# Kernel tuning notes

Hardware: AMD Instinct MI355X
Metric: run time of the kernel (lower is better)

Reference implementation:

```python
import jax, jax.numpy as jnp
import numpy as np

N = 131072
MANO_CHILD = (2, 3, 17, 5, 6, 18, 8, 9, 20, 11, 12, 19, 14, 15, 16)
MANO_PARENT = (1, 2, 3, 4, 5, 6, 7, 8, 9, 10, 11, 12, 13, 14, 15)
FINGERS = ((0, 1, 2, 3, 17), (0, 4, 5, 6, 18), (0, 7, 8, 9, 20), (0, 10, 11, 12, 19), (0, 13, 14, 15, 16))
PALM = np.array([0, 1, 4, 7, 10, 13])
MAX_FLEX = float(np.pi / 2)  # flexion clamp range [0, pi/2]
EPS = 1e-8


def _wrist_rot(src, dst):
    """Kabsch rotation R (N,3,3) such that R @ src_k ~= dst_k (palm alignment)."""
    H = jnp.einsum('nki,nkj->nij', src, dst)          # sum_k src dst^T
    U, S, Vt = jnp.linalg.svd(H, full_matrices=False)
    VUt = jnp.einsum('nji,nkj->nik', Vt, U)           # V @ U^T
    d = jnp.linalg.det(VUt)
    D = jnp.stack([jnp.ones_like(d), jnp.ones_like(d), d], axis=-1)
    return jnp.einsum('nji,nj,nkj->nik', Vt, D, U)    # V diag(1,1,d) U^T


def _rodrigues(v, axis, theta):
    """Rotate vectors v (N,3) about unit axis (N,3) by angle theta (N,)."""
    c = jnp.cos(theta)[:, None]
    s = jnp.sin(theta)[:, None]
    return v * c + jnp.cross(axis, v) * s + axis * jnp.sum(axis * v, -1, keepdims=True) * (1.0 - c)


def _forward(joints, tempJ):
    wrist = joints[:, :1]
    J = joints - wrist                       # wrist-centered observed joints
    T = tempJ - tempJ[:, :1]                 # wrist-centered template
    bone_ref = T                             # bonelenTempJ: reference bone lengths
    # rigid palm alignment of template onto observed joints
    R = _wrist_rot(T[:, PALM], J[:, PALM])
    T = jnp.einsum('nij,nkj->nki', R, T)     # rotate every template joint
    # palm joints of observation are replaced by aligned template palm
    J = J.at[:, PALM].set(T[:, PALM])
    # (hand-pose-legitimize layer approximated as identity; source unavailable)
    for idx in range(len(MANO_CHILD)):
        ch, pa = MANO_CHILD[idx], MANO_PARENT[idx]
        v1 = J[:, ch] - T[:, pa]
        dis = jnp.linalg.norm(v1, axis=1)
        univ1 = v1 / (dis[:, None] + EPS)
        blen = jnp.linalg.norm(bone_ref[:, ch] - bone_ref[:, pa], axis=1)
        lo, hi = blen, blen                  # non-RHD template: lower == upper
        valid = (lo <= dis) & (dis <= hi)
        clamped = jnp.clip(dis, lo, hi)
        new = jnp.where(valid[:, None], J[:, ch], T[:, pa] + univ1 * clamped[:, None])
        T = T.at[:, ch].set(new)
        # flexion legitimization: clamp bend angle of this bone vs its parent bone
        f = FINGERS[idx // 3]
        k = idx % 3
        gp, pp, cc = f[k], f[k + 1], f[k + 2]  # grandparent, parent(=pa), child(=ch)
        v0 = T[:, pp] - T[:, gp]
        vb = T[:, cc] - T[:, pp]
        cr = jnp.cross(v0, vb)
        s = jnp.linalg.norm(cr, axis=1)
        c = jnp.sum(v0 * vb, axis=1)
        ang = jnp.arctan2(s, c)
        delta = jnp.clip(ang, 0.0, MAX_FLEX) - ang
        axis = cr / (s[:, None] + EPS)
        T = T.at[:, cc].set(_rodrigues(vb, axis, delta) + T[:, pp])
    return wrist + T


def setup_inputs() -> dict:
    key = jax.random.key(0)
    k1, k2 = jax.random.split(key)
    joints = jax.random.normal(k1, (N, 21, 3), dtype=jnp.float32)
    tempJ = jax.random.normal(k2, (N, 21, 3), dtype=jnp.float32)
    return {"joints": joints, "tempJ": tempJ}


def reference(joints, tempJ):
    return _forward(joints, tempJ)
```

## Files before the change

### kernel.cpp

```cpp
#include <hip/hip_runtime.h>
#include <math.h>

#define KEPS 1e-8f

__global__ __launch_bounds__(256)
void kin_fwd(const float* __restrict__ joints,
             const float* __restrict__ tempJ,
             float* __restrict__ out,
             int n_total)
{
    constexpr int CHILD[15]  = {2,3,17, 5,6,18, 8,9,20, 11,12,19, 14,15,16};
    constexpr int PARENT[15] = {1,2,3, 4,5,6, 7,8,9, 10,11,12, 13,14,15};
    constexpr int GPID[15]   = {0,1,2, 0,4,5, 0,7,8, 0,10,11, 0,13,14};
    constexpr int PALM[6]    = {0,1,4,7,10,13};

    const int n = blockIdx.x * blockDim.x + threadIdx.x;
    if (n >= n_total) return;

    const float* jp = joints + (long long)n * 63;
    const float* tp = tempJ  + (long long)n * 63;

    float Jl[21][3], T[21][3];
#pragma unroll
    for (int k = 0; k < 21; ++k) {
        Jl[k][0] = jp[3*k+0];
        Jl[k][1] = jp[3*k+1];
        Jl[k][2] = jp[3*k+2];
    }
    const float wx = Jl[0][0], wy = Jl[0][1], wz = Jl[0][2];
#pragma unroll
    for (int k = 0; k < 21; ++k) { Jl[k][0] -= wx; Jl[k][1] -= wy; Jl[k][2] -= wz; }

#pragma unroll
    for (int k = 0; k < 21; ++k) {
        T[k][0] = tp[3*k+0];
        T[k][1] = tp[3*k+1];
        T[k][2] = tp[3*k+2];
    }
    const float ox = T[0][0], oy = T[0][1], oz = T[0][2];
#pragma unroll
    for (int k = 0; k < 21; ++k) { T[k][0] -= ox; T[k][1] -= oy; T[k][2] -= oz; }

    float blen[15];
#pragma unroll
    for (int i = 0; i < 15; ++i) {
        const float dx = T[CHILD[i]][0] - T[PARENT[i]][0];
        const float dy = T[CHILD[i]][1] - T[PARENT[i]][1];
        const float dz = T[CHILD[i]][2] - T[PARENT[i]][2];
        blen[i] = sqrtf(dx*dx + dy*dy + dz*dz);
    }

    float H[3][3] = {{0.f,0.f,0.f},{0.f,0.f,0.f},{0.f,0.f,0.f}};
#pragma unroll
    for (int p = 0; p < 6; ++p) {
        const int k = PALM[p];
#pragma unroll
        for (int i = 0; i < 3; ++i)
#pragma unroll
            for (int j = 0; j < 3; ++j)
                H[i][j] += T[k][i] * Jl[k][j];
    }

    float A[3][3];
#pragma unroll
    for (int i = 0; i < 3; ++i)
#pragma unroll
        for (int j = 0; j < 3; ++j)
            A[i][j] = H[0][i]*H[0][j] + H[1][i]*H[1][j] + H[2][i]*H[2][j];

    float V[3][3] = {{1.f,0.f,0.f},{0.f,1.f,0.f},{0.f,0.f,1.f}};
#pragma unroll
    for (int sw = 0; sw < 6; ++sw) {
#pragma unroll
        for (int r = 0; r < 3; ++r) {
            const int p = (r == 2) ? 1 : 0;
            const int q = (r == 0) ? 1 : 2;
            const float b   = A[p][q];
            const float dif = A[q][q] - A[p][p];
            const float rho = sqrtf(dif*dif + 4.f*b*b);
            const float c2  = (rho > 0.f) ? (dif / rho) : 1.f;
            const float c   = sqrtf(fmaxf(0.5f*(1.f + c2), 0.f));
            const float s   = copysignf(sqrtf(fmaxf(0.5f*(1.f - c2), 0.f)), b);
#pragma unroll
            for (int i = 0; i < 3; ++i) {
                const float aip = A[i][p], aiq = A[i][q];
                A[i][p] = c*aip - s*aiq;
                A[i][q] = s*aip + c*aiq;
            }
#pragma unroll
            for (int j = 0; j < 3; ++j) {
                const float apj = A[p][j], aqj = A[q][j];
                A[p][j] = c*apj - s*aqj;
                A[q][j] = s*apj + c*aqj;
            }
#pragma unroll
            for (int i = 0; i < 3; ++i) {
                const float vip = V[i][p], viq = V[i][q];
                V[i][p] = c*vip - s*viq;
                V[i][q] = s*vip + c*viq;
            }
        }
    }

    float lam[3] = {A[0][0], A[1][1], A[2][2]};
#pragma unroll
    for (int pass = 0; pass < 3; ++pass) {
        const int i = (pass == 2) ? 1 : 0;
        const int j = (pass == 0) ? 1 : 2;
        if (lam[i] < lam[j]) {
            const float tl = lam[i]; lam[i] = lam[j]; lam[j] = tl;
#pragma unroll
            for (int r2 = 0; r2 < 3; ++r2) {
                const float tv = V[r2][i]; V[r2][i] = V[r2][j]; V[r2][j] = tv;
            }
        }
    }

    float R[3][3];
    {
        const float v1x = V[0][0], v1y = V[1][0], v1z = V[2][0];
        const float v2x = V[0][1], v2y = V[1][1], v2z = V[2][1];
        const float v3x = V[0][2], v3y = V[1][2], v3z = V[2][2];

        float w1x = H[0][0]*v1x + H[0][1]*v1y + H[0][2]*v1z;
        float w1y = H[1][0]*v1x + H[1][1]*v1y + H[1][2]*v1z;
        float w1z = H[2][0]*v1x + H[2][1]*v1y + H[2][2]*v1z;
        const float n1 = sqrtf(w1x*w1x + w1y*w1y + w1z*w1z);
        const float in1 = 1.f / fmaxf(n1, 1e-20f);
        const float u1x = w1x*in1, u1y = w1y*in1, u1z = w1z*in1;

        float w2x = H[0][0]*v2x + H[0][1]*v2y + H[0][2]*v2z;
        float w2y = H[1][0]*v2x + H[1][1]*v2y + H[1][2]*v2z;
        float w2z = H[2][0]*v2x + H[2][1]*v2y + H[2][2]*v2z;
        const float dp = u1x*w2x + u1y*w2y + u1z*w2z;
        w2x -= dp*u1x; w2y -= dp*u1y; w2z -= dp*u1z;
        const float n2 = sqrtf(w2x*w2x + w2y*w2y + w2z*w2z);
        const float in2 = 1.f / fmaxf(n2, 1e-20f);
        const float u2x = w2x*in2, u2y = w2y*in2, u2z = w2z*in2;

        const float u3x = u1y*u2z - u1z*u2y;
        const float u3y = u1z*u2x - u1x*u2z;
        const float u3z = u1x*u2y - u1y*u2x;

        const float detV =
            v1x*(v2y*v3z - v2z*v3y) - v1y*(v2x*v3z - v2z*v3x) + v1z*(v2x*v3y - v2y*v3x);
        const float d = (detV < 0.f) ? -1.f : 1.f;
        const float w3x = d*v3x, w3y = d*v3y, w3z = d*v3z;

        R[0][0] = v1x*u1x + v2x*u2x + w3x*u3x;
        R[0][1] = v1x*u1y + v2x*u2y + w3x*u3y;
        R[0][2] = v1x*u1z + v2x*u2z + w3x*u3z;
        R[1][0] = v1y*u1x + v2y*u2x + w3y*u3x;
        R[1][1] = v1y*u1y + v2y*u2y + w3y*u3y;
        R[1][2] = v1y*u1z + v2y*u2z + w3y*u3z;
        R[2][0] = v1z*u1x + v2z*u2x + w3z*u3x;
        R[2][1] = v1z*u1y + v2z*u2y + w3z*u3y;
        R[2][2] = v1z*u1z + v2z*u2z + w3z*u3z;
    }

#pragma unroll
    for (int k = 0; k < 21; ++k) {
        const float x = T[k][0], y = T[k][1], z = T[k][2];
        T[k][0] = R[0][0]*x + R[0][1]*y + R[0][2]*z;
        T[k][1] = R[1][0]*x + R[1][1]*y + R[1][2]*z;
        T[k][2] = R[2][0]*x + R[2][1]*y + R[2][2]*z;
    }

#pragma unroll
    for (int i = 0; i < 15; ++i) {
        const int ch = CHILD[i], pa = PARENT[i], gp = GPID[i];

        const float v1x = Jl[ch][0] - T[pa][0];
        const float v1y = Jl[ch][1] - T[pa][1];
        const float v1z = Jl[ch][2] - T[pa][2];
        const float dis = sqrtf(v1x*v1x + v1y*v1y + v1z*v1z);
        const float bl  = blen[i];
        const float sc  = bl / (dis + KEPS);
        const bool valid = (dis == bl);
        T[ch][0] = valid ? Jl[ch][0] : T[pa][0] + v1x*sc;
        T[ch][1] = valid ? Jl[ch][1] : T[pa][1] + v1y*sc;
        T[ch][2] = valid ? Jl[ch][2] : T[pa][2] + v1z*sc;

        const float v0x = T[pa][0] - T[gp][0];
        const float v0y = T[pa][1] - T[gp][1];
        const float v0z = T[pa][2] - T[gp][2];
        const float vbx = T[ch][0] - T[pa][0];
        const float vby = T[ch][1] - T[pa][1];
        const float vbz = T[ch][2] - T[pa][2];

        const float crx = v0y*vbz - v0z*vby;
        const float cry = v0z*vbx - v0x*vbz;
        const float crz = v0x*vby - v0y*vbx;
        const float s2  = crx*crx + cry*cry + crz*crz;
        const float s   = sqrtf(s2);
        const float c   = v0x*vbx + v0y*vby + v0z*vbz;

        const float rlen = sqrtf(s2 + c*c);
        const float invr = 1.f / fmaxf(rlen, 1e-30f);
        const float cosd = (c < 0.f) ? s*invr : 1.f;
        const float sind = (c < 0.f) ? c*invr : 0.f;

        const float sainv = 1.f / (s + KEPS);
        const float ax = crx*sainv, ay = cry*sainv, az = crz*sainv;

        const float cxx = ay*vbz - az*vby;
        const float cxy = az*vbx - ax*vbz;
        const float cxz = ax*vby - ay*vbx;
        const float adv = ax*vbx + ay*vby + az*vbz;
        const float omc = 1.f - cosd;
        T[ch][0] = vbx*cosd + cxx*sind + ax*adv*omc + T[pa][0];
        T[ch][1] = vby*cosd + cxy*sind + ay*adv*omc + T[pa][1];
        T[ch][2] = vbz*cosd + cxz*sind + az*adv*omc + T[pa][2];
    }

    float* op = out + (long long)n * 63;
#pragma unroll
    for (int k = 0; k < 21; ++k) {
        op[3*k+0] = wx + T[k][0];
        op[3*k+1] = wy + T[k][1];
        op[3*k+2] = wz + T[k][2];
    }
}

extern "C" void kernel_launch(void* const* d_in, const int* in_sizes, int n_in,
                              void* d_out, int out_size, void* d_ws, size_t ws_size,
                              hipStream_t stream)
{
    const float* joints = (const float*)d_in[0];
    const float* tempJ  = (const float*)d_in[1];
    float* out          = (float*)d_out;

    const int n_total = in_sizes[0] / 63;
    const int block = 256;
    const int grid  = (n_total + block - 1) / block;
    kin_fwd<<<grid, block, 0, stream>>>(joints, tempJ, out, n_total);
}
```

Baseline: 125.9 us.

## Stage inputs and outputs through shared memory with coalesced float4 copies

Each block now copies its tile of tempJ and then joints from global memory into LDS with coalesced float4 loads, and threads read their 63-float records from LDS. Outputs are written back to LDS and stored with coalesced float4 writes. This replaces the strided per-thread 63-float accesses, which coalesce poorly. In exchange it adds about 64KB of LDS per block, which limits occupancy, plus several barriers. The stride-63 LDS reads may also cause bank conflicts.

```diff
diff --git a/kernel.cpp b/kernel.cpp
--- a/kernel.cpp
+++ b/kernel.cpp
@@ -2,8 +2,12 @@
 #include <math.h>
 
 #define KEPS 1e-8f
-
-__global__ __launch_bounds__(256)
+#define BLOCK 256
+#define HF 63
+#define TILE_F (BLOCK * HF)
+#define TILE_V4 (TILE_F / 4)
+
+__global__ __launch_bounds__(BLOCK)
 void kin_fwd(const float* __restrict__ joints,
              const float* __restrict__ tempJ,
              float* __restrict__ out,
@@ -14,211 +18,269 @@
     constexpr int GPID[15]   = {0,1,2, 0,4,5, 0,7,8, 0,10,11, 0,13,14};
     constexpr int PALM[6]    = {0,1,4,7,10,13};
 
-    const int n = blockIdx.x * blockDim.x + threadIdx.x;
-    if (n >= n_total) return;
-
-    const float* jp = joints + (long long)n * 63;
-    const float* tp = tempJ  + (long long)n * 63;
-
-    float Jl[21][3], T[21][3];
-#pragma unroll
-    for (int k = 0; k < 21; ++k) {
-        Jl[k][0] = jp[3*k+0];
-        Jl[k][1] = jp[3*k+1];
-        Jl[k][2] = jp[3*k+2];
-    }
-    const float wx = Jl[0][0], wy = Jl[0][1], wz = Jl[0][2];
-#pragma unroll
-    for (int k = 0; k < 21; ++k) { Jl[k][0] -= wx; Jl[k][1] -= wy; Jl[k][2] -= wz; }
-
-#pragma unroll
-    for (int k = 0; k < 21; ++k) {
-        T[k][0] = tp[3*k+0];
-        T[k][1] = tp[3*k+1];
-        T[k][2] = tp[3*k+2];
-    }
-    const float ox = T[0][0], oy = T[0][1], oz = T[0][2];
-#pragma unroll
-    for (int k = 0; k < 21; ++k) { T[k][0] -= ox; T[k][1] -= oy; T[k][2] -= oz; }
-
+    __shared__ float lds[TILE_F];
+
+    const int tid = threadIdx.x;
+    const int n   = blockIdx.x * BLOCK + tid;
+    const long long tileBase = (long long)blockIdx.x * TILE_F;
+    const long long totalF   = (long long)n_total * HF;
+    const bool fullTile = (tileBase + TILE_F) <= totalF;
+
+    if (fullTile) {
+        const float4* g4 = (const float4*)(tempJ + tileBase);
+        float4* l4 = (float4*)lds;
+#pragma unroll
+        for (int r = 0; r < TILE_V4; r += BLOCK) {
+            const int idx = r + tid;
+            if (idx < TILE_V4) l4[idx] = g4[idx];
+        }
+    } else {
+        for (int idx = tid; idx < TILE_F; idx += BLOCK) {
+            const long long g = tileBase + idx;
+            lds[idx] = (g < totalF) ? tempJ[g] : 0.f;
+        }
+    }
+    __syncthreads();
+
+    const bool active = (n < n_total);
+    float T[21][3];
     float blen[15];
-#pragma unroll
-    for (int i = 0; i < 15; ++i) {
-        const float dx = T[CHILD[i]][0] - T[PARENT[i]][0];
-        const float dy = T[CHILD[i]][1] - T[PARENT[i]][1];
-        const float dz = T[CHILD[i]][2] - T[PARENT[i]][2];
-        blen[i] = sqrtf(dx*dx + dy*dy + dz*dz);
-    }
-
-    float H[3][3] = {{0.f,0.f,0.f},{0.f,0.f,0.f},{0.f,0.f,0.f}};
-#pragma unroll
-    for (int p = 0; p < 6; ++p) {
-        const int k = PALM[p];
+    float wx = 0.f, wy = 0.f, wz = 0.f;
+
+    if (active) {
+        const float* tl = lds + tid * HF;
+#pragma unroll
+        for (int k = 0; k < 21; ++k) {
+            T[k][0] = tl[3*k+0];
+            T[k][1] = tl[3*k+1];
+            T[k][2] = tl[3*k+2];
+        }
+        const float ox = T[0][0], oy = T[0][1], oz = T[0][2];
+#pragma unroll
+        for (int k = 0; k < 21; ++k) { T[k][0] -= ox; T[k][1] -= oy; T[k][2] -= oz; }
+
+#pragma unroll
+        for (int i = 0; i < 15; ++i) {
+            const float dx = T[CHILD[i]][0] - T[PARENT[i]][0];
+            const float dy = T[CHILD[i]][1] - T[PARENT[i]][1];
+            const float dz = T[CHILD[i]][2] - T[PARENT[i]][2];
+            blen[i] = sqrtf(dx*dx + dy*dy + dz*dz);
+        }
+    }
+    __syncthreads();
+
+    if (fullTile) {
+        const float4* g4 = (const float4*)(joints + tileBase);
+        float4* l4 = (float4*)lds;
+#pragma unroll
+        for (int r = 0; r < TILE_V4; r += BLOCK) {
+            const int idx = r + tid;
+            if (idx < TILE_V4) l4[idx] = g4[idx];
+        }
+    } else {
+        for (int idx = tid; idx < TILE_F; idx += BLOCK) {
+            const long long g = tileBase + idx;
+            lds[idx] = (g < totalF) ? joints[g] : 0.f;
+        }
+    }
+    __syncthreads();
+
+    if (active) {
+        const float* jl = lds + tid * HF;
+        wx = jl[0]; wy = jl[1]; wz = jl[2];
+
+        #define JLC(k,d) (jl[3*(k)+(d)] - ((d)==0 ? wx : ((d)==1 ? wy : wz)))
+
+        float H[3][3] = {{0.f,0.f,0.f},{0.f,0.f,0.f},{0.f,0.f,0.f}};
+#pragma unroll
+        for (int p = 0; p < 6; ++p) {
+            const int k = PALM[p];
+            const float jx = JLC(k,0), jy = JLC(k,1), jz = JLC(k,2);
+            H[0][0] += T[k][0]*jx; H[0][1] += T[k][0]*jy; H[0][2] += T[k][0]*jz;
+            H[1][0] += T[k][1]*jx; H[1][1] += T[k][1]*jy; H[1][2] += T[k][1]*jz;
+            H[2][0] += T[k][2]*jx; H[2][1] += T[k][2]*jy; H[2][2] += T[k][2]*jz;
+        }
+
+        float A[3][3];
 #pragma unroll
         for (int i = 0; i < 3; ++i)
 #pragma unroll
             for (int j = 0; j < 3; ++j)
-                H[i][j] += T[k][i] * Jl[k][j];
-    }
-
-    float A[3][3];
-#pragma unroll
-    for (int i = 0; i < 3; ++i)
-#pragma unroll
-        for (int j = 0; j < 3; ++j)
-            A[i][j] = H[0][i]*H[0][j] + H[1][i]*H[1][j] + H[2][i]*H[2][j];
-
-    float V[3][3] = {{1.f,0.f,0.f},{0.f,1.f,0.f},{0.f,0.f,1.f}};
-#pragma unroll
-    for (int sw = 0; sw < 6; ++sw) {
-#pragma unroll
-        for (int r = 0; r < 3; ++r) {
-            const int p = (r == 2) ? 1 : 0;
-            const int q = (r == 0) ? 1 : 2;
-            const float b   = A[p][q];
-            const float dif = A[q][q] - A[p][p];
-            const float rho = sqrtf(dif*dif + 4.f*b*b);
-            const float c2  = (rho > 0.f) ? (dif / rho) : 1.f;
-            const float c   = sqrtf(fmaxf(0.5f*(1.f + c2), 0.f));
-            const float s   = copysignf(sqrtf(fmaxf(0.5f*(1.f - c2), 0.f)), b);
-#pragma unroll
-            for (int i = 0; i < 3; ++i) {
-                const float aip = A[i][p], aiq = A[i][q];
-                A[i][p] = c*aip - s*aiq;
-                A[i][q] = s*aip + c*aiq;
+                A[i][j] = H[0][i]*H[0][j] + H[1][i]*H[1][j] + H[2][i]*H[2][j];
+
+        float V[3][3] = {{1.f,0.f,0.f},{0.f,1.f,0.f},{0.f,0.f,1.f}};
+#pragma unroll
+        for (int sw = 0; sw < 6; ++sw) {
+#pragma unroll
+            for (int r = 0; r < 3; ++r) {
+                const int p = (r == 2) ? 1 : 0;
+                const int q = (r == 0) ? 1 : 2;
+                const float b   = A[p][q];
+                const float dif = A[q][q] - A[p][p];
+                const float rho = sqrtf(dif*dif + 4.f*b*b);
+                const float c2  = (rho > 0.f) ? (dif / rho) : 1.f;
+                const float c   = sqrtf(fmaxf(0.5f*(1.f + c2), 0.f));
+                const float s   = copysignf(sqrtf(fmaxf(0.5f*(1.f - c2), 0.f)), b);
+#pragma unroll
+                for (int i = 0; i < 3; ++i) {
+                    const float aip = A[i][p], aiq = A[i][q];
+                    A[i][p] = c*aip - s*aiq;
+                    A[i][q] = s*aip + c*aiq;
+                }
+#pragma unroll
+                for (int j = 0; j < 3; ++j) {
+                    const float apj = A[p][j], aqj = A[q][j];
+                    A[p][j] = c*apj - s*aqj;
+                    A[q][j] = s*apj + c*aqj;
+                }
+#pragma unroll
+                for (int i = 0; i < 3; ++i) {
+                    const float vip = V[i][p], viq = V[i][q];
+                    V[i][p] = c*vip - s*viq;
+                    V[i][q] = s*vip + c*viq;
+                }
             }
-#pragma unroll
-            for (int j = 0; j < 3; ++j) {
-                const float apj = A[p][j], aqj = A[q][j];
-                A[p][j] = c*apj - s*aqj;
-                A[q][j] = s*apj + c*aqj;
+        }
+
+        float lam[3] = {A[0][0], A[1][1], A[2][2]};
+#pragma unroll
+        for (int pass = 0; pass < 3; ++pass) {
+            const int i = (pass == 2) ? 1 : 0;
+            const int j = (pass == 0) ? 1 : 2;
+            if (lam[i] < lam[j]) {
+                const float tl2 = lam[i]; lam[i] = lam[j]; lam[j] = tl2;
+#pragma unroll
+                for (int r2 = 0; r2 < 3; ++r2) {
+                    const float tv = V[r2][i]; V[r2][i] = V[r2][j]; V[r2][j] = tv;
+                }
             }
-#pragma unroll
-            for (int i = 0; i < 3; ++i) {
-                const float vip = V[i][p], viq = V[i][q];
-                V[i][p] = c*vip - s*viq;
-                V[i][q] = s*vip + c*viq;
-            }
-        }
-    }
-
-    float lam[3] = {A[0][0], A[1][1], A[2][2]};
-#pragma unroll
-    for (int pass = 0; pass < 3; ++pass) {
-        const int i = (pass == 2) ? 1 : 0;
-        const int j = (pass == 0) ? 1 : 2;
-        if (lam[i] < lam[j]) {
-            const float tl = lam[i]; lam[i] = lam[j]; lam[j] = tl;
-#pragma unroll
-            for (int r2 = 0; r2 < 3; ++r2) {
-                const float tv = V[r2][i]; V[r2][i] = V[r2][j]; V[r2][j] = tv;
-            }
-        }
-    }
-
-    float R[3][3];
-    {
-        const float v1x = V[0][0], v1y = V[1][0], v1z = V[2][0];
-        const float v2x = V[0][1], v2y = V[1][1], v2z = V[2][1];
-        const float v3x = V[0][2], v3y = V[1][2], v3z = V[2][2];
-
-        float w1x = H[0][0]*v1x + H[0][1]*v1y + H[0][2]*v1z;
-        float w1y = H[1][0]*v1x + H[1][1]*v1y + H[1][2]*v1z;
-        float w1z = H[2][0]*v1x + H[2][1]*v1y + H[2][2]*v1z;
-        const float n1 = sqrtf(w1x*w1x + w1y*w1y + w1z*w1z);
-        const float in1 = 1.f / fmaxf(n1, 1e-20f);
-        const float u1x = w1x*in1, u1y = w1y*in1, u1z = w1z*in1;
-
-        float w2x = H[0][0]*v2x + H[0][1]*v2y + H[0][2]*v2z;
-        float w2y = H[1][0]*v2x + H[1][1]*v2y + H[1][2]*v2z;
-        float w2z = H[2][0]*v2x + H[2][1]*v2y + H[2][2]*v2z;
-        const float dp = u1x*w2x + u1y*w2y + u1z*w2z;
-        w2x -= dp*u1x; w2y -= dp*u1y; w2z -= dp*u1z;
-        const float n2 = sqrtf(w2x*w2x + w2y*w2y + w2z*w2z);
-        const float in2 = 1.f / fmaxf(n2, 1e-20f);
-        const float u2x = w2x*in2, u2y = w2y*in2, u2z = w2z*in2;
-
-        const float u3x = u1y*u2z - u1z*u2y;
-        const float u3y = u1z*u2x - u1x*u2z;
-        const float u3z = u1x*u2y - u1y*u2x;
-
-        const float detV =
-            v1x*(v2y*v3z - v2z*v3y) - v1y*(v2x*v3z - v2z*v3x) + v1z*(v2x*v3y - v2y*v3x);
-        const float d = (detV < 0.f) ? -1.f : 1.f;
-        const float w3x = d*v3x, w3y = d*v3y, w3z = d*v3z;
-
-        R[0][0] = v1x*u1x + v2x*u2x + w3x*u3x;
-        R[0][1] = v1x*u1y + v2x*u2y + w3x*u3y;
-        R[0][2] = v1x*u1z + v2x*u2z + w3x*u3z;
-        R[1][0] = v1y*u1x + v2y*u2x + w3y*u3x;
-        R[1][1] = v1y*u1y + v2y*u2y + w3y*u3y;
-        R[1][2] = v1y*u1z + v2y*u2z + w3y*u3z;
-        R[2][0] = v1z*u1x + v2z*u2x + w3z*u3x;
-        R[2][1] = v1z*u1y + v2z*u2y + w3z*u3y;
-        R[2][2] = v1z*u1z + v2z*u2z + w3z*u3z;
-    }
-
-#pragma unroll
-    for (int k = 0; k < 21; ++k) {
-        const float x = T[k][0], y = T[k][1], z = T[k][2];
-        T[k][0] = R[0][0]*x + R[0][1]*y + R[0][2]*z;
-        T[k][1] = R[1][0]*x + R[1][1]*y + R[1][2]*z;
-        T[k][2] = R[2][0]*x + R[2][1]*y + R[2][2]*z;
-    }
-
-#pragma unroll
-    for (int i = 0; i < 15; ++i) {
-        const int ch = CHILD[i], pa = PARENT[i], gp = GPID[i];
-
-        const float v1x = Jl[ch][0] - T[pa][0];
-        const float v1y = Jl[ch][1] - T[pa][1];
-        const float v1z = Jl[ch][2] - T[pa][2];
-        const float dis = sqrtf(v1x*v1x + v1y*v1y + v1z*v1z);
-        const float bl  = blen[i];
-        const float sc  = bl / (dis + KEPS);
-        const bool valid = (dis == bl);
-        T[ch][0] = valid ? Jl[ch][0] : T[pa][0] + v1x*sc;
-        T[ch][1] = valid ? Jl[ch][1] : T[pa][1] + v1y*sc;
-        T[ch][2] = valid ? Jl[ch][2] : T[pa][2] + v1z*sc;
-
-        const float v0x = T[pa][0] - T[gp][0];
-        const float v0y = T[pa][1] - T[gp][1];
-        const float v0z = T[pa][2] - T[gp][2];
-        const float vbx = T[ch][0] - T[pa][0];
-        const float vby = T[ch][1] - T[pa][1];
-        const float vbz = T[ch][2] - T[pa][2];
-
-        const float crx = v0y*vbz - v0z*vby;
-        const float cry = v0z*vbx - v0x*vbz;
-        const float crz = v0x*vby - v0y*vbx;
-        const float s2  = crx*crx + cry*cry + crz*crz;
-        const float s   = sqrtf(s2);
-        const float c   = v0x*vbx + v0y*vby + v0z*vbz;
-
-        const float rlen = sqrtf(s2 + c*c);
-        const float invr = 1.f / fmaxf(rlen, 1e-30f);
-        const float cosd = (c < 0.f) ? s*invr : 1.f;
-        const float sind = (c < 0.f) ? c*invr : 0.f;
-
-        const float sainv = 1.f / (s + KEPS);
-        const float ax = crx*sainv, ay = cry*sainv, az = crz*sainv;
-
-        const float cxx = ay*vbz - az*vby;
-        const float cxy = az*vbx - ax*vbz;
-        const float cxz = ax*vby - ay*vbx;
-        const float adv = ax*vbx + ay*vby + az*vbz;
-        const float omc = 1.f - cosd;
-        T[ch][0] = vbx*cosd + cxx*sind + ax*adv*omc + T[pa][0];
-        T[ch][1] = vby*cosd + cxy*sind + ay*adv*omc + T[pa][1];
-        T[ch][2] = vbz*cosd + cxz*sind + az*adv*omc + T[pa][2];
-    }
-
-    float* op = out + (long long)n * 63;
-#pragma unroll
-    for (int k = 0; k < 21; ++k) {
-        op[3*k+0] = wx + T[k][0];
-        op[3*k+1] = wy + T[k][1];
-        op[3*k+2] = wz + T[k][2];
+        }
+
+        float R[3][3];
+        {
+            const float v1x = V[0][0], v1y = V[1][0], v1z = V[2][0];
+            const float v2x = V[0][1], v2y = V[1][1], v2z = V[2][1];
+            const float v3x = V[0][2], v3y = V[1][2], v3z = V[2][2];
+
+            float w1x = H[0][0]*v1x + H[0][1]*v1y + H[0][2]*v1z;
+            float w1y = H[1][0]*v1x + H[1][1]*v1y + H[1][2]*v1z;
+            float w1z = H[2][0]*v1x + H[2][1]*v1y + H[2][2]*v1z;
+            const float n1 = sqrtf(w1x*w1x + w1y*w1y + w1z*w1z);
+            const float in1 = 1.f / fmaxf(n1, 1e-20f);
+            const float u1x = w1x*in1, u1y = w1y*in1, u1z = w1z*in1;
+
+            float w2x = H[0][0]*v2x + H[0][1]*v2y + H[0][2]*v2z;
+            float w2y = H[1][0]*v2x + H[1][1]*v2y + H[1][2]*v2z;
+            float w2z = H[2][0]*v2x + H[2][1]*v2y + H[2][2]*v2z;
+            const float dp = u1x*w2x + u1y*w2y + u1z*w2z;
+            w2x -= dp*u1x; w2y -= dp*u1y; w2z -= dp*u1z;
+            const float n2 = sqrtf(w2x*w2x + w2y*w2y + w2z*w2z);
+            const float in2 = 1.f / fmaxf(n2, 1e-20f);
+            const float u2x = w2x*in2, u2y = w2y*in2, u2z = w2z*in2;
+
+            const float u3x = u1y*u2z - u1z*u2y;
+            const float u3y = u1z*u2x - u1x*u2z;
+            const float u3z = u1x*u2y - u1y*u2x;
+
+            const float detV =
+                v1x*(v2y*v3z - v2z*v3y) - v1y*(v2x*v3z - v2z*v3x) + v1z*(v2x*v3y - v2y*v3x);
+            const float d = (detV < 0.f) ? -1.f : 1.f;
+            const float w3x = d*v3x, w3y = d*v3y, w3z = d*v3z;
+
+            R[0][0] = v1x*u1x + v2x*u2x + w3x*u3x;
+            R[0][1] = v1x*u1y + v2x*u2y + w3x*u3y;
+            R[0][2] = v1x*u1z + v2x*u2z + w3x*u3z;
+            R[1][0] = v1y*u1x + v2y*u2x + w3y*u3x;
+            R[1][1] = v1y*u1y + v2y*u2y + w3y*u3y;
+            R[1][2] = v1y*u1z + v2y*u2z + w3y*u3z;
+            R[2][0] = v1z*u1x + v2z*u2x + w3z*u3x;
+            R[2][1] = v1z*u1y + v2z*u2y + w3z*u3y;
+            R[2][2] = v1z*u1z + v2z*u2z + w3z*u3z;
+        }
+
+#pragma unroll
+        for (int k = 0; k < 21; ++k) {
+            const float x = T[k][0], y = T[k][1], z = T[k][2];
+            T[k][0] = R[0][0]*x + R[0][1]*y + R[0][2]*z;
+            T[k][1] = R[1][0]*x + R[1][1]*y + R[1][2]*z;
+            T[k][2] = R[2][0]*x + R[2][1]*y + R[2][2]*z;
+        }
+
+#pragma unroll
+        for (int i = 0; i < 15; ++i) {
+            const int ch = CHILD[i], pa = PARENT[i], gp = GPID[i];
+
+            const float jcx = JLC(ch,0), jcy = JLC(ch,1), jcz = JLC(ch,2);
+            const float v1x = jcx - T[pa][0];
+            const float v1y = jcy - T[pa][1];
+            const float v1z = jcz - T[pa][2];
+            const float dis = sqrtf(v1x*v1x + v1y*v1y + v1z*v1z);
+            const float bl  = blen[i];
+            const float sc  = bl / (dis + KEPS);
+            const bool valid = (dis == bl);
+            T[ch][0] = valid ? jcx : T[pa][0] + v1x*sc;
+            T[ch][1] = valid ? jcy : T[pa][1] + v1y*sc;
+            T[ch][2] = valid ? jcz : T[pa][2] + v1z*sc;
+
+            const float v0x = T[pa][0] - T[gp][0];
+            const float v0y = T[pa][1] - T[gp][1];
+            const float v0z = T[pa][2] - T[gp][2];
+            const float vbx = T[ch][0] - T[pa][0];
+            const float vby = T[ch][1] - T[pa][1];
+            const float vbz = T[ch][2] - T[pa][2];
+
+            const float crx = v0y*vbz - v0z*vby;
+            const float cry = v0z*vbx - v0x*vbz;
+            const float crz = v0x*vby - v0y*vbx;
+            const float s2  = crx*crx + cry*cry + crz*crz;
+            const float s   = sqrtf(s2);
+            const float c   = v0x*vbx + v0y*vby + v0z*vbz;
+
+            const float rlen = sqrtf(s2 + c*c);
+            const float invr = 1.f / fmaxf(rlen, 1e-30f);
+            const float cosd = (c < 0.f) ? s*invr : 1.f;
+            const float sind = (c < 0.f) ? c*invr : 0.f;
+
+            const float sainv = 1.f / (s + KEPS);
+            const float ax = crx*sainv, ay = cry*sainv, az = crz*sainv;
+
+            const float cxx = ay*vbz - az*vby;
+            const float cxy = az*vbx - ax*vbz;
+            const float cxz = ax*vby - ay*vbx;
+            const float adv = ax*vbx + ay*vby + az*vbz;
+            const float omc = 1.f - cosd;
+            T[ch][0] = vbx*cosd + cxx*sind + ax*adv*omc + T[pa][0];
+            T[ch][1] = vby*cosd + cxy*sind + ay*adv*omc + T[pa][1];
+            T[ch][2] = vbz*cosd + cxz*sind + az*adv*omc + T[pa][2];
+        }
+        #undef JLC
+    }
+    __syncthreads();
+
+    if (active) {
+        float* ol = lds + tid * HF;
+#pragma unroll
+        for (int k = 0; k < 21; ++k) {
+            ol[3*k+0] = wx + T[k][0];
+            ol[3*k+1] = wy + T[k][1];
+            ol[3*k+2] = wz + T[k][2];
+        }
+    }
+    __syncthreads();
+
+    if (fullTile) {
+        float4* g4 = (float4*)(out + tileBase);
+        const float4* l4 = (const float4*)lds;
+#pragma unroll
+        for (int r = 0; r < TILE_V4; r += BLOCK) {
+            const int idx = r + tid;
+            if (idx < TILE_V4) g4[idx] = l4[idx];
+        }
+    } else {
+        for (int idx = tid; idx < TILE_F; idx += BLOCK) {
+            const long long g = tileBase + idx;
+            if (g < totalF) out[g] = lds[idx];
+        }
     }
 }
 
@@ -231,7 +293,6 @@
     float* out          = (float*)d_out;
 
     const int n_total = in_sizes[0] / 63;
-    const int block = 256;
-    const int grid  = (n_total + block - 1) / block;
-    kin_fwd<<<grid, block, 0, stream>>>(joints, tempJ, out, n_total);
+    const int grid = (n_total + BLOCK - 1) / BLOCK;
+    kin_fwd<<<grid, BLOCK, 0, stream>>>(joints, tempJ, out, n_total);
 }
```

Measured after the change: 117.1 us. 1.07x faster.
